# Optimization experiments

Hardware: AMD Instinct MI355X
Metric: run time of the kernel (lower is better)

Reference implementation:

```python
import jax, jax.numpy as jnp
import numpy as np

SHAPES = [(64, 64), (32, 32), (16, 16), (8, 8)]  # (H, W) per level, sum HW = 5440
DIMS, NH, NLVL, NPTS, D_HEIGHT, NCAM, NQ, BS = 256, 8, 4, 8, 4, 6, 10000, 1


def ms_deform_attn(value, shapes, loc, attw):
    # value [B, sumHW, nH, dh]; loc [B, nq, nH, L, P, 2] in [0,1]; attw [B, nq, nH, L, P]
    B, _, nH, dh = value.shape
    nq, P = loc.shape[1], loc.shape[4]
    out = jnp.zeros((B, nH, nq, dh), value.dtype)
    start = 0
    for lvl, (h, w) in enumerate(shapes):
        v = value[:, start:start + h * w].transpose(0, 2, 1, 3)  # [B,nH,hw,dh]
        start += h * w
        l = loc[:, :, :, lvl].transpose(0, 2, 1, 3, 4)  # [B,nH,nq,P,2]
        x = l[..., 0] * w - 0.5
        y = l[..., 1] * h - 0.5
        x0, y0 = jnp.floor(x), jnp.floor(y)
        acc = jnp.zeros((B, nH, nq, P, dh), value.dtype)
        for dy in (0.0, 1.0):
            for dx in (0.0, 1.0):
                cx, cy = x0 + dx, y0 + dy
                wgt = (1.0 - jnp.abs(x - cx)) * (1.0 - jnp.abs(y - cy))
                valid = (cx >= 0) & (cx < w) & (cy >= 0) & (cy < h)
                xi = jnp.clip(cx, 0, w - 1).astype(jnp.int32)
                yi = jnp.clip(cy, 0, h - 1).astype(jnp.int32)
                idx = (yi * w + xi).reshape(B, nH, -1)  # [B,nH,nq*P]
                g = jnp.take_along_axis(v, idx[..., None], axis=2).reshape(B, nH, nq, P, dh)
                acc = acc + jnp.where(valid, wgt, 0.0)[..., None] * g
        aw = attw[:, :, :, lvl].transpose(0, 2, 1, 3)  # [B,nH,nq,P]
        out = out + jnp.einsum('bhqp,bhqpd->bhqd', aw, acc)
    return out.transpose(0, 2, 1, 3).reshape(B, nq, nH * dh)


def setup_inputs() -> dict:
    key = jax.random.key(0)
    ks = jax.random.split(key, 16)
    l = sum(h * w for h, w in SHAPES)
    s = 1.0 / np.sqrt(DIMS)
    inp = {
        'query': jax.random.normal(ks[0], (BS, NQ, DIMS), jnp.float32),
        'key': jax.random.normal(ks[1], (NCAM, l, BS, DIMS), jnp.float32),
        'value': jax.random.normal(ks[2], (NCAM, l, BS, DIMS), jnp.float32),
        'ref_points': jax.random.uniform(ks[3], (NCAM, BS, NQ, D_HEIGHT, 2), jnp.float32),
        'vox_mask': jax.random.randint(ks[4], (NCAM, BS, NQ, D_HEIGHT), 0, 2) > 0,
        'spatial_shapes': np.array(SHAPES, dtype=np.int64),
        'level_start_index': np.array([0, 4096, 5120, 5376], dtype=np.int64),
        'value_W': jax.random.uniform(ks[5], (DIMS, DIMS), jnp.float32, -s, s),
        'value_b': jnp.zeros((DIMS,), jnp.float32),
        'off_W': jax.random.normal(ks[6], (DIMS, NH * NLVL * NPTS * 2), jnp.float32) * 0.01,
        'off_b': jax.random.normal(ks[7], (NH * NLVL * NPTS * 2,), jnp.float32) * 0.1,
        'attw_W': jax.random.normal(ks[8], (DIMS, NH * NLVL * NPTS), jnp.float32) * 0.02,
        'attw_b': jnp.zeros((NH * NLVL * NPTS,), jnp.float32),
        'out_W': jax.random.uniform(ks[9], (DIMS, DIMS), jnp.float32, -s, s),
        'out_b': jnp.zeros((DIMS,), jnp.float32),
    }
    return inp


def reference(query, key, value, ref_points, vox_mask, spatial_shapes, level_start_index,
              value_W, value_b, off_W, off_b, attw_W, attw_b, out_W, out_b):
    shapes = [(int(h), int(w)) for h, w in np.asarray(spatial_shapes)]
    bs, nq, dims = query.shape
    cam = vox_mask.shape[0]
    B = bs * cam
    nH = NH
    dh = dims // nH
    Lv, P, D = len(shapes), NPTS, ref_points.shape[3]

    # value_proj; key unused by deformable attention math
    v = value.transpose(2, 0, 1, 3).reshape(B, -1, dims)
    v = (v @ value_W + value_b).reshape(B, -1, nH, dh)

    # rebatch: every camera sees the full (batch-0 visible) query set; padded
    # entries in the original are discarded, so computing all and masking is exact.
    q = jnp.broadcast_to(query[:, None], (bs, cam, nq, dims)).reshape(B, nq, dims)

    off = (q @ off_W + off_b).reshape(B, nq, nH, Lv, P, 2)
    attw = jax.nn.softmax((q @ attw_W + attw_b).reshape(B, nq, nH, Lv * P), -1)
    attw = attw.reshape(B, nq, nH, Lv, P)

    norm = jnp.array([[w, h] for h, w in shapes], q.dtype)  # [Lv,2] -> (W,H)
    off = off / norm[None, None, None, :, None, :]

    ref_rb = ref_points.transpose(1, 0, 2, 3, 4).reshape(B, nq, D, 2)
    off = off.reshape(B, nq, nH, Lv, P // D, D, 2)
    loc = (ref_rb[:, :, None, None, None] + off).reshape(B, nq, nH, Lv, P, 2)

    out = ms_deform_attn(v, shapes, loc, attw).reshape(bs, cam, nq, dims)

    valid = (vox_mask[:, 0].sum(-1) > 0).astype(q.dtype)  # [cam,nq] (batch-0 indexes, as original)
    slots = jnp.einsum('cq,bcqd->bqd', valid, out)
    count = (vox_mask.sum(-1) > 0).transpose(1, 2, 0).sum(-1).astype(q.dtype)
    count = jnp.maximum(count, 1.0)
    slots = slots / count[..., None]
    slots = slots @ out_W + out_b
    return slots + query  # dropout = identity (eval); inp_residual = query
```

## Files before the change

kernel.cpp:

```cpp
#include <hip/hip_runtime.h>


typedef unsigned short ushort_t;
typedef unsigned int uint_t;
typedef __attribute__((ext_vector_type(8))) short bf16x8;
typedef __attribute__((ext_vector_type(4))) float f32x4;
typedef __attribute__((ext_vector_type(2))) _Float16 f16x2;

__device__ __forceinline__ float bf2f(ushort_t u) {
    return __uint_as_float(((uint_t)u) << 16);
}
__device__ __forceinline__ ushort_t f2bf(float f) {
    uint_t i = __float_as_uint(f);
    uint_t r = i + 0x7fffu + ((i >> 16) & 1u);
    return (ushort_t)(r >> 16);
}
__device__ __forceinline__ bf16x8 pack8(float4 v0, float4 v1) {
    union { uint_t u[4]; bf16x8 v; } r;
    asm("v_cvt_pk_bf16_f32 %0, %1, %2" : "=v"(r.u[0]) : "v"(v0.x), "v"(v0.y));
    asm("v_cvt_pk_bf16_f32 %0, %1, %2" : "=v"(r.u[1]) : "v"(v0.z), "v"(v0.w));
    asm("v_cvt_pk_bf16_f32 %0, %1, %2" : "=v"(r.u[2]) : "v"(v1.x), "v"(v1.y));
    asm("v_cvt_pk_bf16_f32 %0, %1, %2" : "=v"(r.u[3]) : "v"(v1.z), "v"(v1.w));
    return r.v;
}
__device__ __forceinline__ ushort_t f2h(float f) {
    union { _Float16 h; ushort_t u; } cv;
    cv.h = (_Float16)f;
    return cv.u;
}

__device__ __forceinline__ void pk_fma8(uint_t* a, uint_t wp, const uint4& v) {
    asm("v_pk_fma_f16 %0, %1, %2, %0" : "+v"(a[0]) : "v"(wp), "v"(v.x));
    asm("v_pk_fma_f16 %0, %1, %2, %0" : "+v"(a[1]) : "v"(wp), "v"(v.y));
    asm("v_pk_fma_f16 %0, %1, %2, %0" : "+v"(a[2]) : "v"(wp), "v"(v.z));
    asm("v_pk_fma_f16 %0, %1, %2, %0" : "+v"(a[3]) : "v"(wp), "v"(v.w));
}

__global__ __launch_bounds__(256) void prep_w(
    const float* __restrict__ Wv, const float* __restrict__ Wo,
    const float* __restrict__ Wf, const float* __restrict__ Wa,
    ushort_t* __restrict__ Tv, ushort_t* __restrict__ To,
    ushort_t* __restrict__ Tqk) {
    const int z = blockIdx.z;
    const float* W;
    ushort_t* T;
    int N;
    if (z == 0)      { W = Wv; T = Tv;              N = 256; }
    else if (z == 1) { W = Wo; T = To;              N = 256; }
    else if (z == 2) { W = Wf; T = Tqk;             N = 512; }
    else             { W = Wa; T = Tqk + 512 * 256; N = 256; }
    const int n0 = blockIdx.y * 32;
    if (n0 >= N) return;
    const int k0 = blockIdx.x * 32;

    __shared__ float tile[32][33];
    const int tx = threadIdx.x & 31;
    const int ty = threadIdx.x >> 5;
    #pragma unroll
    for (int r = 0; r < 4; ++r) {
        const int k = ty + r * 8;
        tile[k][tx] = W[(size_t)(k0 + k) * N + n0 + tx];
    }
    __syncthreads();
    #pragma unroll
    for (int r = 0; r < 4; ++r) {
        const int n = ty + r * 8;
        T[(size_t)(n0 + n) * 256 + k0 + tx] = f2bf(tile[tx][n]);
    }
}

template <bool AF32, int OUT_MODE, bool RESID>
__device__ __forceinline__ void gemm_body(
    ushort_t (*sA)[128][32], ushort_t (*sB)[128][32],
    const void* __restrict__ Av, int Astride, const ushort_t* __restrict__ Wt,
    const float* __restrict__ bias0, const float* __restrict__ bias1, int split,
    const float* __restrict__ resid, void* __restrict__ Cv,
    int M, int N, int bx, int by) {
    const int m0 = bx * 128;
    const int n0 = by * 128;
    const int t    = threadIdx.x;
    const int lane = t & 63;
    const int w    = t >> 6;
    const int wr   = w >> 1, wc = w & 1;

    const int srow = t >> 2;
    const int skof = (t & 3) * 8;

    const bool am0 = (m0 + srow) < M;
    const bool am1 = (m0 + 64 + srow) < M;
    const float*    Af0 = (const float*)Av + (size_t)(m0 + srow) * Astride + skof;
    const float*    Af1 = Af0 + (size_t)64 * Astride;
    const ushort_t* Ab0 = (const ushort_t*)Av + (size_t)(m0 + srow) * Astride + skof;
    const ushort_t* Ab1 = Ab0 + (size_t)64 * Astride;
    const ushort_t* Bp0 = Wt + (size_t)(n0 + srow) * 256 + skof;
    const ushort_t* Bp1 = Bp0 + (size_t)64 * 256;

    const bf16x8 zz = {0, 0, 0, 0, 0, 0, 0, 0};

    auto loadA = [&](const float* af, const ushort_t* ab, int ko, bool ok) -> bf16x8 {
        if (!ok) return zz;
        if (AF32) {
            const float4 v0 = *(const float4*)(af + ko);
            const float4 v1 = *(const float4*)(af + ko + 4);
            return pack8(v0, v1);
        }
        return *(const bf16x8*)(ab + ko);
    };

    f32x4 acc[4][4];
    #pragma unroll
    for (int i = 0; i < 4; ++i)
        #pragma unroll
        for (int j = 0; j < 4; ++j)
            acc[i][j] = (f32x4){0.f, 0.f, 0.f, 0.f};

    {
        const bf16x8 a0 = loadA(Af0, Ab0, 0, am0);
        const bf16x8 a1 = loadA(Af1, Ab1, 0, am1);
        const bf16x8 b0 = *(const bf16x8*)(Bp0);
        const bf16x8 b1 = *(const bf16x8*)(Bp1);
        *(bf16x8*)(&sA[0][srow][skof])      = a0;
        *(bf16x8*)(&sA[0][64 + srow][skof]) = a1;
        *(bf16x8*)(&sB[0][srow][skof])      = b0;
        *(bf16x8*)(&sB[0][64 + srow][skof]) = b1;
    }
    __syncthreads();

    const int rl = lane & 15;
    const int kq = (lane >> 4) * 8;

    for (int k = 0; k < 8; ++k) {
        const int buf = k & 1;

        bf16x8 na0 = zz, na1 = zz, nb0 = zz, nb1 = zz;
        if (k < 7) {
            const int ko = (k + 1) * 32;
            na0 = loadA(Af0, Ab0, ko, am0);
            na1 = loadA(Af1, Ab1, ko, am1);
            nb0 = *(const bf16x8*)(Bp0 + ko);
            nb1 = *(const bf16x8*)(Bp1 + ko);
        }

        bf16x8 af[4], bfr[4];
        #pragma unroll
        for (int i = 0; i < 4; ++i)
            af[i] = *(const bf16x8*)(&sA[buf][wr * 64 + i * 16 + rl][kq]);
        #pragma unroll
        for (int j = 0; j < 4; ++j)
            bfr[j] = *(const bf16x8*)(&sB[buf][wc * 64 + j * 16 + rl][kq]);
        #pragma unroll
        for (int i = 0; i < 4; ++i)
            #pragma unroll
            for (int j = 0; j < 4; ++j)
                acc[i][j] = __builtin_amdgcn_mfma_f32_16x16x32_bf16(
                    af[i], bfr[j], acc[i][j], 0, 0, 0);

        if (k < 7) {
            __syncthreads();
            *(bf16x8*)(&sA[buf ^ 1][srow][skof])      = na0;
            *(bf16x8*)(&sA[buf ^ 1][64 + srow][skof]) = na1;
            *(bf16x8*)(&sB[buf ^ 1][srow][skof])      = nb0;
            *(bf16x8*)(&sB[buf ^ 1][64 + srow][skof]) = nb1;
            __syncthreads();
        }
    }

    const int col_l = lane & 15;
    const int rq    = (lane >> 4) * 4;
    #pragma unroll
    for (int j = 0; j < 4; ++j) {
        const int gn = n0 + wc * 64 + j * 16 + col_l;
        const float bj = (gn < split) ? bias0[gn] : bias1[gn - split];
        #pragma unroll
        for (int i = 0; i < 4; ++i) {
            #pragma unroll
            for (int r = 0; r < 4; ++r) {
                const int gm = m0 + wr * 64 + i * 16 + rq + r;
                if (gm >= M) continue;
                float v = acc[i][j][r] + bj;
                if (RESID) v += resid[(size_t)gm * N + gn];
                if (OUT_MODE == 1)
                    ((ushort_t*)Cv)[(size_t)gm * N + gn] = f2bf(v);
                else if (OUT_MODE == 2)
                    ((ushort_t*)Cv)[(size_t)gm * N + gn] = f2h(v);
                else
                    ((float*)Cv)[(size_t)gm * N + gn] = v;
            }
        }
    }
}

__global__ __launch_bounds__(256) void gemm_vqk(
    const float* __restrict__ value, const ushort_t* __restrict__ value_Wt,
    const float* __restrict__ value_b, ushort_t* __restrict__ vproj,
    const float* __restrict__ query, const ushort_t* __restrict__ qk_Wt,
    const float* __restrict__ off_b, const float* __restrict__ attw_b,
    ushort_t* __restrict__ qkcat) {
    __shared__ ushort_t sA[2][128][32];
    __shared__ ushort_t sB[2][128][32];
    int b = blockIdx.x;
    if (b < 510) {
        gemm_body<true, 2, false>(sA, sB, value, 256, value_Wt, value_b,
                                  value_b, 256, nullptr, (void*)vproj,
                                  32640, 256, b % 255, b / 255);
    } else {
        b -= 510;
        gemm_body<true, 1, false>(sA, sB, query, 256, qk_Wt, off_b, attw_b,
                                  512, nullptr, (void*)qkcat, 10000, 768,
                                  b % 79, b / 79);
    }
}

__global__ __launch_bounds__(256) void gemm_out_k(
    const ushort_t* __restrict__ slots,
    const ushort_t* __restrict__ out_Wt,
    const float* __restrict__ out_b, const float* __restrict__ query,
    float* __restrict__ out) {
    __shared__ ushort_t sA[2][128][32];
    __shared__ ushort_t sB[2][128][32];
    gemm_body<false, 0, true>(sA, sB, slots, 768, out_Wt, out_b, out_b, 256,
                              query, (void*)out, 10000, 256,
                              blockIdx.x, blockIdx.y);
}

__global__ __launch_bounds__(128) void sample_k(
    ushort_t* __restrict__ qkcat,
    const float* __restrict__ refp,
    const int* __restrict__ vox,
    const ushort_t* __restrict__ vproj) {
    const int q    = blockIdx.x;
    const int hb   = blockIdx.y << 2;
    const int tid  = threadIdx.x;
    const int lane = tid & 63;
    const int h    = hb + (tid >> 5);
    const int lp   = tid & 31;
    const int slice = (tid >> 2) & 7;
    const int g     = tid & 3;

    int mm = 0;
    if (lane < 6) {
        const uint4 vm = *(const uint4*)(vox + ((lane * 10000 + q) << 2));
        mm = (int)(vm.x | vm.y | vm.z | vm.w);
    }
    float sv[6];
    #pragma unroll
    for (int c = 0; c < 6; ++c) sv[c] = __shfl(mm, c) ? 1.0f : 0.0f;
    const float cnt = sv[0] + sv[1] + sv[2] + sv[3] + sv[4] + sv[5];

    const float a = bf2f(qkcat[(size_t)q * 768 + 512 + h * 32 + lp]);
    float mx = a;
    #pragma unroll
    for (int o = 16; o >= 1; o >>= 1) mx = fmaxf(mx, __shfl_xor(mx, o));
    const float e = __expf(a - mx);
    float se = e;
    #pragma unroll
    for (int o = 16; o >= 1; o >>= 1) se += __shfl_xor(se, o);
    const float aw = e / se;

    const int lvl = lp >> 3;
    const int p   = lp & 7;
    const int dd  = p & 3;
    const int   Sarr[4]   = {64, 32, 16, 8};
    const int   Lstart[4] = {0, 4096, 5120, 5376};
    const int   S  = Sarr[lvl];
    const float Sf = (float)S;
    const int   lstart = Lstart[lvl];
    const int   hoff   = h << 6;
    const float ox = bf2f(qkcat[(size_t)q * 768 + h * 64 + lvl * 16 + p * 2 + 0]) / Sf;
    const float oy = bf2f(qkcat[(size_t)q * 768 + h * 64 + lvl * 16 + p * 2 + 1]) / Sf;

    float acc[8] = {0.f, 0.f, 0.f, 0.f, 0.f, 0.f, 0.f, 0.f};
    const char* vpb = (const char*)vproj;
    const int goff = g << 4;
    const int srcbase = (lane & 32) + slice * 4;

    for (int c = 0; c < 6; ++c) {
        if (sv[c] == 0.0f) continue;

        int    cb[4];
        uint_t cwp[4];
        {
            const int cbase = c * 5440 + lstart;
            const int rbase = ((c * 10000 + q) * 4 + dd) * 2;
            const float rx = refp[rbase + 0];
            const float ry = refp[rbase + 1];
            const float x  = (rx + ox) * Sf - 0.5f;
            const float y  = (ry + oy) * Sf - 0.5f;
            const float x0 = floorf(x), y0 = floorf(y);
            #pragma unroll
            for (int k = 0; k < 4; ++k) {
                const float cx = x0 + (float)(k & 1);
                const float cy = y0 + (float)(k >> 1);
                const float wgt = (1.0f - fabsf(x - cx)) * (1.0f - fabsf(y - cy));
                const bool ok = (cx >= 0.0f) & (cx < Sf) & (cy >= 0.0f) & (cy < Sf);
                const int xi = (int)fminf(fmaxf(cx, 0.0f), Sf - 1.0f);
                const int yi = (int)fminf(fmaxf(cy, 0.0f), Sf - 1.0f);
                cb[k] = ((cbase + yi * S + xi) << 9) + hoff;
                const float cw = ok ? wgt * aw : 0.0f;
                const uint_t hw = (uint_t)f2h(cw);
                cwp[k] = (hw << 16) | hw;
            }
        }

        int b[4][4];
        #pragma unroll
        for (int j = 0; j < 4; ++j) {
            const int src = srcbase + j;
            b[j][0] = __shfl(cb[0], src);
            b[j][1] = __shfl(cb[1], src);
            b[j][2] = __shfl(cb[2], src);
            b[j][3] = __shfl(cb[3], src);
        }

        uint_t acch[4] = {0u, 0u, 0u, 0u};
        uint4 v0 = *(const uint4*)(vpb + (b[0][0] + goff));
        uint4 v1 = *(const uint4*)(vpb + (b[0][1] + goff));
        uint4 v2 = *(const uint4*)(vpb + (b[0][2] + goff));
        uint4 v3 = *(const uint4*)(vpb + (b[0][3] + goff));
        #pragma unroll
        for (int j = 0; j < 4; ++j) {
            uint4 n0 = v0, n1 = v1, n2 = v2, n3 = v3;
            if (j < 3) {
                n0 = *(const uint4*)(vpb + (b[j + 1][0] + goff));
                n1 = *(const uint4*)(vpb + (b[j + 1][1] + goff));
                n2 = *(const uint4*)(vpb + (b[j + 1][2] + goff));
                n3 = *(const uint4*)(vpb + (b[j + 1][3] + goff));
            }
            const int src = srcbase + j;
            const uint_t w0 = (uint_t)__shfl((int)cwp[0], src);
            const uint_t w1 = (uint_t)__shfl((int)cwp[1], src);
            const uint_t w2 = (uint_t)__shfl((int)cwp[2], src);
            const uint_t w3 = (uint_t)__shfl((int)cwp[3], src);
            pk_fma8(acch, w0, v0);
            pk_fma8(acch, w1, v1);
            pk_fma8(acch, w2, v2);
            pk_fma8(acch, w3, v3);
            v0 = n0; v1 = n1; v2 = n2; v3 = n3;
        }

        #pragma unroll
        for (int n = 0; n < 4; ++n) {
            union { uint_t u; f16x2 h; } cvu;
            cvu.u = acch[n];
            acc[2 * n]     += (float)cvu.h.x;
            acc[2 * n + 1] += (float)cvu.h.y;
        }
    }

    #pragma unroll
    for (int n = 0; n < 8; ++n) {
        acc[n] += __shfl_xor(acc[n], 4);
        acc[n] += __shfl_xor(acc[n], 8);
        acc[n] += __shfl_xor(acc[n], 16);
    }

    if (slice == 0) {
        const float inv = 1.0f / fmaxf(cnt, 1.0f);
        uint4 r;
        asm("v_cvt_pk_bf16_f32 %0, %1, %2"
            : "=v"(r.x) : "v"(acc[0] * inv), "v"(acc[1] * inv));
        asm("v_cvt_pk_bf16_f32 %0, %1, %2"
            : "=v"(r.y) : "v"(acc[2] * inv), "v"(acc[3] * inv));
        asm("v_cvt_pk_bf16_f32 %0, %1, %2"
            : "=v"(r.z) : "v"(acc[4] * inv), "v"(acc[5] * inv));
        asm("v_cvt_pk_bf16_f32 %0, %1, %2"
            : "=v"(r.w) : "v"(acc[6] * inv), "v"(acc[7] * inv));
        *(uint4*)(&qkcat[(size_t)q * 768 + 512 + h * 32 + g * 8]) = r;
    }
}

extern "C" void kernel_launch(void* const* d_in, const int* in_sizes, int n_in,
                              void* d_out, int out_size, void* d_ws, size_t ws_size,
                              hipStream_t stream) {
    const float* query   = (const float*)d_in[0];
    const float* value   = (const float*)d_in[2];
    const float* refp    = (const float*)d_in[3];
    const int*   vox     = (const int*)d_in[4];
    const float* value_W = (const float*)d_in[7];
    const float* value_b = (const float*)d_in[8];
    const float* off_W   = (const float*)d_in[9];
    const float* off_b   = (const float*)d_in[10];
    const float* attw_W  = (const float*)d_in[11];
    const float* attw_b  = (const float*)d_in[12];
    const float* out_W   = (const float*)d_in[13];
    const float* out_b   = (const float*)d_in[14];
    float* out = (float*)d_out;

    char* ws = (char*)d_ws;
    ushort_t* vproj    = (ushort_t*)ws;
    ushort_t* qkcat    = (ushort_t*)(ws + 16711680);
    ushort_t* value_Wt = (ushort_t*)(ws + 32071680);
    ushort_t* out_Wt   = (ushort_t*)(ws + 32071680 + 131072);
    ushort_t* qk_Wt    = (ushort_t*)(ws + 32071680 + 262144);

    prep_w<<<dim3(8, 16, 4), 256, 0, stream>>>(
        value_W, out_W, off_W, attw_W, value_Wt, out_Wt, qk_Wt);
    gemm_vqk<<<984, 256, 0, stream>>>(value, value_Wt, value_b, vproj,
                                      query, qk_Wt, off_b, attw_b, qkcat);
    sample_k<<<dim3(10000, 2), 128, 0, stream>>>(qkcat, refp, vox, vproj);
    gemm_out_k<<<dim3(79, 2), 256, 0, stream>>>(qkcat + 512, out_Wt, out_b,
                                                query, out);
}
```

Before: 325.8 us.

## Replace shared-memory block GEMM with single-wave register-direct GEMM tiles

Each GEMM now runs as a single 64-thread wave computing a 64x64 tile, with A and B fragments loaded straight from global memory into MFMA registers. The LDS staging, double buffering and barriers are gone. The grids grow to 3924 and 628 blocks to keep the GPU busy. In exchange there is less data reuse across waves, so more global/L2 traffic per output, and the out-of-range rows are clamped rather than zero-filled.

New measurement: 346.1 us. 1.06x slower.

```diff
diff --git a/kernel.cpp b/kernel.cpp
--- a/kernel.cpp
+++ b/kernel.cpp
@@ -70,42 +70,30 @@
 }
 
 template <bool AF32, int OUT_MODE, bool RESID>
-__device__ __forceinline__ void gemm_body(
-    ushort_t (*sA)[128][32], ushort_t (*sB)[128][32],
+__device__ __forceinline__ void gemm_wave(
     const void* __restrict__ Av, int Astride, const ushort_t* __restrict__ Wt,
     const float* __restrict__ bias0, const float* __restrict__ bias1, int split,
     const float* __restrict__ resid, void* __restrict__ Cv,
     int M, int N, int bx, int by) {
-    const int m0 = bx * 128;
-    const int n0 = by * 128;
-    const int t    = threadIdx.x;
-    const int lane = t & 63;
-    const int w    = t >> 6;
-    const int wr   = w >> 1, wc = w & 1;
-
-    const int srow = t >> 2;
-    const int skof = (t & 3) * 8;
-
-    const bool am0 = (m0 + srow) < M;
-    const bool am1 = (m0 + 64 + srow) < M;
-    const float*    Af0 = (const float*)Av + (size_t)(m0 + srow) * Astride + skof;
-    const float*    Af1 = Af0 + (size_t)64 * Astride;
-    const ushort_t* Ab0 = (const ushort_t*)Av + (size_t)(m0 + srow) * Astride + skof;
-    const ushort_t* Ab1 = Ab0 + (size_t)64 * Astride;
-    const ushort_t* Bp0 = Wt + (size_t)(n0 + srow) * 256 + skof;
-    const ushort_t* Bp1 = Bp0 + (size_t)64 * 256;
-
-    const bf16x8 zz = {0, 0, 0, 0, 0, 0, 0, 0};
-
-    auto loadA = [&](const float* af, const ushort_t* ab, int ko, bool ok) -> bf16x8 {
-        if (!ok) return zz;
-        if (AF32) {
-            const float4 v0 = *(const float4*)(af + ko);
-            const float4 v1 = *(const float4*)(af + ko + 4);
-            return pack8(v0, v1);
-        }
-        return *(const bf16x8*)(ab + ko);
-    };
+    const int m0 = bx * 64;
+    const int n0 = by * 64;
+    const int lane = threadIdx.x & 63;
+    const int rl = lane & 15;
+    const int kq = (lane >> 4) * 8;
+
+    const float*    Afp[4];
+    const ushort_t* Abp[4];
+    const ushort_t* Bp[4];
+    #pragma unroll
+    for (int i = 0; i < 4; ++i) {
+        int gm = m0 + i * 16 + rl;
+        if (gm > M - 1) gm = M - 1;
+        Afp[i] = (const float*)Av + (size_t)gm * Astride + kq;
+        Abp[i] = (const ushort_t*)Av + (size_t)gm * Astride + kq;
+    }
+    #pragma unroll
+    for (int j = 0; j < 4; ++j)
+        Bp[j] = Wt + (size_t)(n0 + j * 16 + rl) * 256 + kq;
 
     f32x4 acc[4][4];
     #pragma unroll
@@ -114,68 +102,39 @@
         for (int j = 0; j < 4; ++j)
             acc[i][j] = (f32x4){0.f, 0.f, 0.f, 0.f};
 
-    {
-        const bf16x8 a0 = loadA(Af0, Ab0, 0, am0);
-        const bf16x8 a1 = loadA(Af1, Ab1, 0, am1);
-        const bf16x8 b0 = *(const bf16x8*)(Bp0);
-        const bf16x8 b1 = *(const bf16x8*)(Bp1);
-        *(bf16x8*)(&sA[0][srow][skof])      = a0;
-        *(bf16x8*)(&sA[0][64 + srow][skof]) = a1;
-        *(bf16x8*)(&sB[0][srow][skof])      = b0;
-        *(bf16x8*)(&sB[0][64 + srow][skof]) = b1;
-    }
-    __syncthreads();
-
-    const int rl = lane & 15;
-    const int kq = (lane >> 4) * 8;
-
-    for (int k = 0; k < 8; ++k) {
-        const int buf = k & 1;
-
-        bf16x8 na0 = zz, na1 = zz, nb0 = zz, nb1 = zz;
-        if (k < 7) {
-            const int ko = (k + 1) * 32;
-            na0 = loadA(Af0, Ab0, ko, am0);
-            na1 = loadA(Af1, Ab1, ko, am1);
-            nb0 = *(const bf16x8*)(Bp0 + ko);
-            nb1 = *(const bf16x8*)(Bp1 + ko);
-        }
-
+    #pragma unroll 2
+    for (int k0 = 0; k0 < 256; k0 += 32) {
         bf16x8 af[4], bfr[4];
         #pragma unroll
-        for (int i = 0; i < 4; ++i)
-            af[i] = *(const bf16x8*)(&sA[buf][wr * 64 + i * 16 + rl][kq]);
+        for (int i = 0; i < 4; ++i) {
+            if (AF32)
+                af[i] = pack8(*(const float4*)(Afp[i] + k0),
+                              *(const float4*)(Afp[i] + k0 + 4));
+            else
+                af[i] = *(const bf16x8*)(Abp[i] + k0);
+        }
         #pragma unroll
         for (int j = 0; j < 4; ++j)
-            bfr[j] = *(const bf16x8*)(&sB[buf][wc * 64 + j * 16 + rl][kq]);
+            bfr[j] = *(const bf16x8*)(Bp[j] + k0);
         #pragma unroll
         for (int i = 0; i < 4; ++i)
             #pragma unroll
             for (int j = 0; j < 4; ++j)
                 acc[i][j] = __builtin_amdgcn_mfma_f32_16x16x32_bf16(
                     af[i], bfr[j], acc[i][j], 0, 0, 0);
-
-        if (k < 7) {
-            __syncthreads();
-            *(bf16x8*)(&sA[buf ^ 1][srow][skof])      = na0;
-            *(bf16x8*)(&sA[buf ^ 1][64 + srow][skof]) = na1;
-            *(bf16x8*)(&sB[buf ^ 1][srow][skof])      = nb0;
-            *(bf16x8*)(&sB[buf ^ 1][64 + srow][skof]) = nb1;
-            __syncthreads();
-        }
     }
 
     const int col_l = lane & 15;
     const int rq    = (lane >> 4) * 4;
     #pragma unroll
     for (int j = 0; j < 4; ++j) {
-        const int gn = n0 + wc * 64 + j * 16 + col_l;
+        const int gn = n0 + j * 16 + col_l;
         const float bj = (gn < split) ? bias0[gn] : bias1[gn - split];
         #pragma unroll
         for (int i = 0; i < 4; ++i) {
             #pragma unroll
             for (int r = 0; r < 4; ++r) {
-                const int gm = m0 + wr * 64 + i * 16 + rq + r;
+                const int gm = m0 + i * 16 + rq + r;
                 if (gm >= M) continue;
                 float v = acc[i][j][r] + bj;
                 if (RESID) v += resid[(size_t)gm * N + gn];
@@ -190,37 +149,33 @@
     }
 }
 
-__global__ __launch_bounds__(256) void gemm_vqk(
+__global__ __launch_bounds__(64) void gemm_vqk(
     const float* __restrict__ value, const ushort_t* __restrict__ value_Wt,
     const float* __restrict__ value_b, ushort_t* __restrict__ vproj,
     const float* __restrict__ query, const ushort_t* __restrict__ qk_Wt,
     const float* __restrict__ off_b, const float* __restrict__ attw_b,
     ushort_t* __restrict__ qkcat) {
-    __shared__ ushort_t sA[2][128][32];
-    __shared__ ushort_t sB[2][128][32];
     int b = blockIdx.x;
-    if (b < 510) {
-        gemm_body<true, 2, false>(sA, sB, value, 256, value_Wt, value_b,
-                                  value_b, 256, nullptr, (void*)vproj,
-                                  32640, 256, b % 255, b / 255);
+    if (b < 2040) {
+        gemm_wave<true, 2, false>(value, 256, value_Wt, value_b, value_b, 256,
+                                  nullptr, (void*)vproj, 32640, 256,
+                                  b >> 2, b & 3);
     } else {
-        b -= 510;
-        gemm_body<true, 1, false>(sA, sB, query, 256, qk_Wt, off_b, attw_b,
-                                  512, nullptr, (void*)qkcat, 10000, 768,
-                                  b % 79, b / 79);
-    }
-}
-
-__global__ __launch_bounds__(256) void gemm_out_k(
+        b -= 2040;
+        gemm_wave<true, 1, false>(query, 256, qk_Wt, off_b, attw_b, 512,
+                                  nullptr, (void*)qkcat, 10000, 768,
+                                  b / 12, b % 12);
+    }
+}
+
+__global__ __launch_bounds__(64) void gemm_out_k(
     const ushort_t* __restrict__ slots,
     const ushort_t* __restrict__ out_Wt,
     const float* __restrict__ out_b, const float* __restrict__ query,
     float* __restrict__ out) {
-    __shared__ ushort_t sA[2][128][32];
-    __shared__ ushort_t sB[2][128][32];
-    gemm_body<false, 0, true>(sA, sB, slots, 768, out_Wt, out_b, out_b, 256,
-                              query, (void*)out, 10000, 256,
-                              blockIdx.x, blockIdx.y);
+    const int b = blockIdx.x;
+    gemm_wave<false, 0, true>(slots, 768, out_Wt, out_b, out_b, 256,
+                              query, (void*)out, 10000, 256, b >> 2, b & 3);
 }
 
 __global__ __launch_bounds__(128) void sample_k(
@@ -395,9 +350,9 @@
 
     prep_w<<<dim3(8, 16, 4), 256, 0, stream>>>(
         value_W, out_W, off_W, attw_W, value_Wt, out_Wt, qk_Wt);
-    gemm_vqk<<<984, 256, 0, stream>>>(value, value_Wt, value_b, vproj,
+    gemm_vqk<<<3924, 64, 0, stream>>>(value, value_Wt, value_b, vproj,
                                       query, qk_Wt, off_b, attw_b, qkcat);
     sample_k<<<dim3(10000, 2), 128, 0, stream>>>(qkcat, refp, vox, vproj);
-    gemm_out_k<<<dim3(79, 2), 256, 0, stream>>>(qkcat + 512, out_Wt, out_b,
-                                                query, out);
-}
+    gemm_out_k<<<628, 64, 0, stream>>>(qkcat + 512, out_Wt, out_b,
+                                       query, out);
+}
```
